# Kernel tuning notes

Hardware: AMD Instinct MI355X
Metric: run time of the kernel (lower is better)

Reference implementation:

```python
import jax, jax.numpy as jnp
import numpy as np

WS = 8
NH = 6

def _ln(x, g, b, eps=1e-5):
    m = jnp.mean(x, axis=-1, keepdims=True)
    v = jnp.var(x, axis=-1, keepdims=True)
    return (x - m) * jax.lax.rsqrt(v + eps) * g + b

def setup_inputs() -> dict:
    key = jax.random.key(0)
    ks = jax.random.split(key, 6)
    B, H, W, C = 4, 256, 256, 192
    s = 0.02
    return {
        "x": jax.random.normal(ks[0], (B, H, W, C), jnp.float32),
        "g1": jnp.ones((C,), jnp.float32),
        "b1": jnp.zeros((C,), jnp.float32),
        "w_qkv": jax.random.normal(ks[1], (C, 3 * C), jnp.float32) * s,
        "b_qkv": jnp.zeros((3 * C,), jnp.float32),
        "w_proj": jax.random.normal(ks[2], (C, C), jnp.float32) * s,
        "b_proj": jnp.zeros((C,), jnp.float32),
        "g2": jnp.ones((C,), jnp.float32),
        "b2": jnp.zeros((C,), jnp.float32),
        "w_fc1": jax.random.normal(ks[3], (C, 4 * C), jnp.float32) * s,
        "b_fc1": jnp.zeros((4 * C,), jnp.float32),
        "w_fc2": jax.random.normal(ks[4], (4 * C, C), jnp.float32) * s,
        "b_fc2": jnp.zeros((C,), jnp.float32),
    }

def reference(x, g1, b1, w_qkv, b_qkv, w_proj, b_proj, g2, b2, w_fc1, b_fc1, w_fc2, b_fc2):
    B, H, W, C = x.shape
    ws, nh = WS, NH
    hd = C // nh
    scale = hd ** -0.5
    N = ws * ws
    # window partition: (B,H,W,C) -> (B*nW, N, C). H,W divisible by ws, so pad branch is a no-op.
    xw = x.reshape(B, H // ws, ws, W // ws, ws, C).transpose(0, 1, 3, 2, 4, 5).reshape(-1, N, C)
    h = _ln(xw, g1, b1)
    qkv = h @ w_qkv + b_qkv                      # (Bn, N, 3C)
    q, k, v = jnp.split(qkv, 3, axis=-1)
    q = q.reshape(-1, N, nh, hd)
    k = k.reshape(-1, N, nh, hd)
    v = v.reshape(-1, N, nh, hd)
    attn = jax.nn.softmax(jnp.einsum('bnhd,bmhd->bhnm', q, k) * scale, axis=-1)
    o = jnp.einsum('bhnm,bmhd->bnhd', attn, v).reshape(-1, N, C)
    xw = xw + (o @ w_proj + b_proj)              # residual inside windows
    # window unpartition: (B*nW, N, C) -> (B, H, W, C)
    xo = xw.reshape(B, H // ws, W // ws, ws, ws, C).transpose(0, 1, 3, 2, 4, 5).reshape(B, H, W, C)
    h2 = _ln(xo, g2, b2)
    h2 = jax.nn.gelu(h2 @ w_fc1 + b_fc1, approximate=False) @ w_fc2 + b_fc2
    return xo + h2
```

## Files before the change

### kernel.cpp

```cpp
#include <hip/hip_runtime.h>
#include <hip/hip_bf16.h>

typedef unsigned short u16;
typedef __attribute__((ext_vector_type(8))) short short8;
typedef __attribute__((ext_vector_type(4))) short short4v;
typedef __attribute__((ext_vector_type(4))) float f32x4;

#define TOK 262144

__device__ __forceinline__ u16 f2bf(float f){
  __hip_bfloat16 h = __float2bfloat16(f);
  return *reinterpret_cast<u16*>(&h);
}

__global__ void transpose_all(const float* __restrict__ w0, u16* __restrict__ d0,
                              const float* __restrict__ w1, u16* __restrict__ d1,
                              const float* __restrict__ w2, u16* __restrict__ d2,
                              const float* __restrict__ w3, u16* __restrict__ d3)
{
  int seg = blockIdx.y;
  const float* s; u16* d; int K, N;
  if      (seg == 0){ s = w0; d = d0; K = 192; N = 576; }
  else if (seg == 1){ s = w1; d = d1; K = 192; N = 192; }
  else if (seg == 2){ s = w2; d = d2; K = 192; N = 768; }
  else              { s = w3; d = d3; K = 768; N = 192; }
  int idx = blockIdx.x * 256 + threadIdx.x;
  if (idx < K * N){
    int k = idx / N, n = idx % N;
    d[n * K + k] = f2bf(s[idx]);
  }
}

__global__ __launch_bounds__(256, 2) void win_attn(
    const float* __restrict__ x,  const float* __restrict__ g1, const float* __restrict__ b1,
    const u16* __restrict__ wqkvT, const float* __restrict__ bqkv,
    const u16* __restrict__ wprojT, const float* __restrict__ bproj,
    float* __restrict__ out)
{
  __shared__ u16 hw[64 * 200];
  __shared__ u16 wch[96 * 200];
  u16* Ql = wch;
  u16* Kl = wch + 64 * 40;
  u16* Vt = Kl  + 64 * 40;
  u16* Pl = Vt  + 32 * 72;

  const int tid = threadIdx.x, lane = tid & 63, w = tid >> 6;
  const int l15 = lane & 15, quad = lane >> 4;
  const int wid = blockIdx.x;
  const int b = wid >> 10, hy = (wid >> 5) & 31, wx = wid & 31;

  {
    int n = w * 16 + (lane >> 2), p = lane & 3;
    int hr = hy * 8 + (n >> 3), wcc = wx * 8 + (n & 7);
    size_t tg = ((size_t)(b * 256 + hr)) * 256 + wcc;
    const float* xr = x + tg * 192 + p * 48;
    float v[48];
    #pragma unroll
    for (int c = 0; c < 12; c++) *(float4*)(v + c * 4) = *(const float4*)(xr + c * 4);
    float s = 0.f, ss = 0.f;
    #pragma unroll
    for (int i = 0; i < 48; i++){ s += v[i]; ss += v[i] * v[i]; }
    s += __shfl_xor(s, 1); ss += __shfl_xor(ss, 1);
    s += __shfl_xor(s, 2); ss += __shfl_xor(ss, 2);
    float m  = s * (1.f / 192.f);
    float rs = rsqrtf(ss * (1.f / 192.f) - m * m + 1e-5f);
    #pragma unroll
    for (int c = 0; c < 12; c++){
      float4 gv = *(const float4*)(g1 + p * 48 + c * 4);
      float4 bv = *(const float4*)(b1 + p * 48 + c * 4);
      short4v t;
      t.x = (short)f2bf((v[c*4+0] - m) * rs * gv.x + bv.x);
      t.y = (short)f2bf((v[c*4+1] - m) * rs * gv.y + bv.y);
      t.z = (short)f2bf((v[c*4+2] - m) * rs * gv.z + bv.z);
      t.w = (short)f2bf((v[c*4+3] - m) * rs * gv.w + bv.w);
      *(short4v*)&hw[n * 200 + p * 48 + c * 4] = t;
    }
  }

  const int qrow = w * 16 + quad * 4;
  f32x4 oall[6][2];
  #pragma unroll
  for (int h = 0; h < 6; h++)
    #pragma unroll
    for (int nt = 0; nt < 2; nt++) oall[h][nt] = (f32x4){0.f, 0.f, 0.f, 0.f};

  #pragma unroll
  for (int head = 0; head < 6; ++head){
    __syncthreads();
    #pragma unroll
    for (int it = 0; it < 9; ++it){
      int c = tid + it * 256;
      int row = c / 24, cc = c % 24;
      int gr = (row >> 5) * 192 + head * 32 + (row & 31);
      *(uint4*)&wch[row * 200 + cc * 8] = *(const uint4*)(wqkvT + (size_t)gr * 192 + cc * 8);
    }
    __syncthreads();
    f32x4 acc[3][2];
    #pragma unroll
    for (int mat = 0; mat < 3; mat++)
      #pragma unroll
      for (int nt = 0; nt < 2; nt++) acc[mat][nt] = (f32x4){0.f, 0.f, 0.f, 0.f};
    #pragma unroll
    for (int k = 0; k < 6; k++){
      short8 af = *(const short8*)&hw[(w * 16 + l15) * 200 + k * 32 + quad * 8];
      #pragma unroll
      for (int mat = 0; mat < 3; mat++)
        #pragma unroll
        for (int nt = 0; nt < 2; nt++){
          short8 bfv = *(const short8*)&wch[(mat * 32 + nt * 16 + l15) * 200 + k * 32 + quad * 8];
          acc[mat][nt] = __builtin_amdgcn_mfma_f32_16x16x32_bf16(af, bfv, acc[mat][nt], 0, 0, 0);
        }
    }
    __syncthreads();
    #pragma unroll
    for (int nt = 0; nt < 2; nt++){
      float bq = bqkv[      head * 32 + nt * 16 + l15];
      float bk = bqkv[192 + head * 32 + nt * 16 + l15];
      float bv = bqkv[384 + head * 32 + nt * 16 + l15];
      #pragma unroll
      for (int r = 0; r < 4; r++){
        Ql[(qrow + r) * 40 + nt * 16 + l15] = f2bf(acc[0][nt][r] + bq);
        Kl[(qrow + r) * 40 + nt * 16 + l15] = f2bf(acc[1][nt][r] + bk);
        Vt[(nt * 16 + l15) * 72 + qrow + r] = f2bf(acc[2][nt][r] + bv);
      }
    }
    __syncthreads();
    short8 aq = *(const short8*)&Ql[(w * 16 + l15) * 40 + quad * 8];
    f32x4 sa[4];
    #pragma unroll
    for (int kt = 0; kt < 4; kt++){
      short8 bk8 = *(const short8*)&Kl[(kt * 16 + l15) * 40 + quad * 8];
      sa[kt] = __builtin_amdgcn_mfma_f32_16x16x32_bf16(aq, bk8, (f32x4){0.f,0.f,0.f,0.f}, 0, 0, 0);
    }
    const float scale = 0.17677669529663687f;
    float inv[4];
    #pragma unroll
    for (int r = 0; r < 4; r++){
      float s0 = sa[0][r] * scale, s1 = sa[1][r] * scale;
      float s2 = sa[2][r] * scale, s3 = sa[3][r] * scale;
      float mx = fmaxf(fmaxf(s0, s1), fmaxf(s2, s3));
      mx = fmaxf(mx, __shfl_xor(mx, 1)); mx = fmaxf(mx, __shfl_xor(mx, 2));
      mx = fmaxf(mx, __shfl_xor(mx, 4)); mx = fmaxf(mx, __shfl_xor(mx, 8));
      float p0 = __expf(s0 - mx), p1 = __expf(s1 - mx);
      float p2 = __expf(s2 - mx), p3 = __expf(s3 - mx);
      float l = p0 + p1 + p2 + p3;
      l += __shfl_xor(l, 1); l += __shfl_xor(l, 2);
      l += __shfl_xor(l, 4); l += __shfl_xor(l, 8);
      inv[r] = 1.f / l;
      Pl[(qrow + r) * 72 +      l15] = f2bf(p0);
      Pl[(qrow + r) * 72 + 16 + l15] = f2bf(p1);
      Pl[(qrow + r) * 72 + 32 + l15] = f2bf(p2);
      Pl[(qrow + r) * 72 + 48 + l15] = f2bf(p3);
    }
    f32x4 oa[2];
    oa[0] = (f32x4){0.f,0.f,0.f,0.f}; oa[1] = (f32x4){0.f,0.f,0.f,0.f};
    #pragma unroll
    for (int ks = 0; ks < 2; ks++){
      short8 ap = *(const short8*)&Pl[(w * 16 + l15) * 72 + ks * 32 + quad * 8];
      #pragma unroll
      for (int nt = 0; nt < 2; nt++){
        short8 bv8 = *(const short8*)&Vt[(nt * 16 + l15) * 72 + ks * 32 + quad * 8];
        oa[nt] = __builtin_amdgcn_mfma_f32_16x16x32_bf16(ap, bv8, oa[nt], 0, 0, 0);
      }
    }
    #pragma unroll
    for (int nt = 0; nt < 2; nt++)
      #pragma unroll
      for (int r = 0; r < 4; r++)
        oall[head][nt][r] = oa[nt][r] * inv[r];
  }

  #pragma unroll
  for (int h = 0; h < 6; h++)
    #pragma unroll
    for (int nt = 0; nt < 2; nt++)
      #pragma unroll
      for (int r = 0; r < 4; r++)
        hw[(qrow + r) * 200 + h * 32 + nt * 16 + l15] = f2bf(oall[h][nt][r]);

  f32x4 accP[12];
  #pragma unroll
  for (int nt = 0; nt < 12; nt++) accP[nt] = (f32x4){0.f,0.f,0.f,0.f};
  #pragma unroll
  for (int k = 0; k < 6; k++){
    short8 af = *(const short8*)&hw[(w * 16 + l15) * 200 + k * 32 + quad * 8];
    #pragma unroll
    for (int nt = 0; nt < 12; nt++){
      short8 bfv = *(const short8*)(wprojT + (size_t)(nt * 16 + l15) * 192 + k * 32 + quad * 8);
      accP[nt] = __builtin_amdgcn_mfma_f32_16x16x32_bf16(af, bfv, accP[nt], 0, 0, 0);
    }
  }
  #pragma unroll
  for (int r = 0; r < 4; r++){
    int nn = qrow + r;
    int hr = hy * 8 + (nn >> 3), wcc = wx * 8 + (nn & 7);
    size_t tg = ((size_t)(b * 256 + hr)) * 256 + wcc;
    #pragma unroll
    for (int nt = 0; nt < 12; nt++){
      int col = nt * 16 + l15;
      size_t idx = tg * 192 + col;
      out[idx] = accP[nt][r] + bproj[col] + x[idx];
    }
  }
}

__global__ __launch_bounds__(256, 2) void mlp_fused(
    const float* __restrict__ g2, const float* __restrict__ b2,
    const u16* __restrict__ wfc1T, const float* __restrict__ bfc1,
    const u16* __restrict__ wfc2T, const float* __restrict__ bfc2,
    float* __restrict__ io)
{
  __shared__ u16 h2t[64 * 200];
  __shared__ u16 Ut[64 * 72];
  __shared__ u16 wcs[192 * 72];

  const int tid = threadIdx.x, lane = tid & 63, w = tid >> 6;
  const int wm = w >> 1, wn = w & 1, l15 = lane & 15, quad = lane >> 4;
  const int t0 = blockIdx.x * 64;

  {
    int n = w * 16 + (lane >> 2), p = lane & 3;
    const float* xr = io + (size_t)(t0 + n) * 192 + p * 48;
    float v[48];
    #pragma unroll
    for (int c = 0; c < 12; c++) *(float4*)(v + c * 4) = *(const float4*)(xr + c * 4);
    float s = 0.f, ss = 0.f;
    #pragma unroll
    for (int i = 0; i < 48; i++){ s += v[i]; ss += v[i] * v[i]; }
    s += __shfl_xor(s, 1); ss += __shfl_xor(ss, 1);
    s += __shfl_xor(s, 2); ss += __shfl_xor(ss, 2);
    float m  = s * (1.f / 192.f);
    float rs = rsqrtf(ss * (1.f / 192.f) - m * m + 1e-5f);
    #pragma unroll
    for (int c = 0; c < 12; c++){
      float4 gv = *(const float4*)(g2 + p * 48 + c * 4);
      float4 bv = *(const float4*)(b2 + p * 48 + c * 4);
      short4v t;
      t.x = (short)f2bf((v[c*4+0] - m) * rs * gv.x + bv.x);
      t.y = (short)f2bf((v[c*4+1] - m) * rs * gv.y + bv.y);
      t.z = (short)f2bf((v[c*4+2] - m) * rs * gv.z + bv.z);
      t.w = (short)f2bf((v[c*4+3] - m) * rs * gv.w + bv.w);
      *(short4v*)&h2t[n * 200 + p * 48 + c * 4] = t;
    }
  }
  __syncthreads();

  f32x4 accO[2][6];
  #pragma unroll
  for (int mt = 0; mt < 2; mt++)
    #pragma unroll
    for (int nt = 0; nt < 6; nt++) accO[mt][nt] = (f32x4){0.f,0.f,0.f,0.f};

  for (int ch = 0; ch < 12; ++ch){
    #pragma unroll
    for (int it = 0; it < 6; ++it){
      int c = tid + it * 256;
      int row = c / 24, cc = c % 24;
      *(uint4*)&wcs[row * 200 + cc * 8] = *(const uint4*)(wfc1T + (size_t)(ch * 64 + row) * 192 + cc * 8);
    }
    __syncthreads();
    f32x4 au[2][2];
    #pragma unroll
    for (int mt = 0; mt < 2; mt++)
      #pragma unroll
      for (int nt = 0; nt < 2; nt++) au[mt][nt] = (f32x4){0.f,0.f,0.f,0.f};
    #pragma unroll
    for (int k = 0; k < 6; k++){
      short8 af0 = *(const short8*)&h2t[(wm * 32 +      l15) * 200 + k * 32 + quad * 8];
      short8 af1 = *(const short8*)&h2t[(wm * 32 + 16 + l15) * 200 + k * 32 + quad * 8];
      #pragma unroll
      for (int nt = 0; nt < 2; nt++){
        short8 bfv = *(const short8*)&wcs[(wn * 32 + nt * 16 + l15) * 200 + k * 32 + quad * 8];
        au[0][nt] = __builtin_amdgcn_mfma_f32_16x16x32_bf16(af0, bfv, au[0][nt], 0, 0, 0);
        au[1][nt] = __builtin_amdgcn_mfma_f32_16x16x32_bf16(af1, bfv, au[1][nt], 0, 0, 0);
      }
    }
    #pragma unroll
    for (int nt = 0; nt < 2; nt++){
      float bb = bfc1[ch * 64 + wn * 32 + nt * 16 + l15];
      #pragma unroll
      for (int mt = 0; mt < 2; mt++)
        #pragma unroll
        for (int r = 0; r < 4; r++){
          float u = au[mt][nt][r] + bb;
          u = 0.5f * u * (1.f + erff(u * 0.70710678118654752f));
          Ut[(wm * 32 + mt * 16 + quad * 4 + r) * 72 + wn * 32 + nt * 16 + l15] = f2bf(u);
        }
    }
    __syncthreads();
    #pragma unroll
    for (int it = 0; it < 6; ++it){
      int c = tid + it * 256;
      int row = c / 8, cc = c % 8;
      *(uint4*)&wcs[row * 72 + cc * 8] = *(const uint4*)(wfc2T + (size_t)row * 768 + ch * 64 + cc * 8);
    }
    __syncthreads();
    #pragma unroll
    for (int ks = 0; ks < 2; ks++){
      short8 af0 = *(const short8*)&Ut[(wm * 32 +      l15) * 72 + ks * 32 + quad * 8];
      short8 af1 = *(const short8*)&Ut[(wm * 32 + 16 + l15) * 72 + ks * 32 + quad * 8];
      #pragma unroll
      for (int nt = 0; nt < 6; nt++){
        short8 bfv = *(const short8*)&wcs[(wn * 96 + nt * 16 + l15) * 72 + ks * 32 + quad * 8];
        accO[0][nt] = __builtin_amdgcn_mfma_f32_16x16x32_bf16(af0, bfv, accO[0][nt], 0, 0, 0);
        accO[1][nt] = __builtin_amdgcn_mfma_f32_16x16x32_bf16(af1, bfv, accO[1][nt], 0, 0, 0);
      }
    }
    __syncthreads();
  }

  #pragma unroll
  for (int mt = 0; mt < 2; mt++)
    #pragma unroll
    for (int nt = 0; nt < 6; nt++){
      int col = wn * 96 + nt * 16 + l15;
      float bb = bfc2[col];
      #pragma unroll
      for (int r = 0; r < 4; r++){
        int row = t0 + wm * 32 + mt * 16 + quad * 4 + r;
        size_t idx = (size_t)row * 192 + col;
        io[idx] = accO[mt][nt][r] + bb + io[idx];
      }
    }
}

extern "C" void kernel_launch(void* const* d_in, const int* in_sizes, int n_in,
                              void* d_out, int out_size, void* d_ws, size_t ws_size,
                              hipStream_t stream) {
  const float* x      = (const float*)d_in[0];
  const float* g1     = (const float*)d_in[1];
  const float* b1     = (const float*)d_in[2];
  const float* w_qkv  = (const float*)d_in[3];
  const float* b_qkv  = (const float*)d_in[4];
  const float* w_proj = (const float*)d_in[5];
  const float* b_proj = (const float*)d_in[6];
  const float* g2     = (const float*)d_in[7];
  const float* b2     = (const float*)d_in[8];
  const float* w_fc1  = (const float*)d_in[9];
  const float* b_fc1  = (const float*)d_in[10];
  const float* w_fc2  = (const float*)d_in[11];
  const float* b_fc2  = (const float*)d_in[12];
  float* out = (float*)d_out;

  u16* wqkvT  = (u16*)d_ws;
  u16* wprojT = wqkvT  + 576 * 192;
  u16* wfc1T  = wprojT + 192 * 192;
  u16* wfc2T  = wfc1T  + 768 * 192;

  transpose_all<<<dim3(576, 4), 256, 0, stream>>>(w_qkv, wqkvT, w_proj, wprojT,
                                                  w_fc1, wfc1T, w_fc2, wfc2T);
  win_attn<<<4096, 256, 0, stream>>>(x, g1, b1, wqkvT, b_qkv, wprojT, b_proj, out);
  mlp_fused<<<4096, 256, 0, stream>>>(g2, b2, wfc1T, b_fc1, wfc2T, b_fc2, out);
}
```

Baseline: 993.4 us.

## Read weight fragments directly from global memory, drop LDS staging, swap erf GELU for tanh approximation

Both the attention and MLP kernels stop staging weight tiles in shared memory and instead load MFMA B-fragments straight from global memory, which relies on L1/L2 caching of the small bf16 weights. This removes the staging copies and several barriers and shrinks LDS use, and launch bounds are raised to 3 and 4 blocks per CU. The exact erf GELU is replaced with a sigmoid-form tanh approximation using exp and a fast reciprocal. The costs are more global load latency in the inner MFMA loops, tighter register limits, and a small numerical deviation from the exact GELU the reference uses.

```diff
diff --git a/kernel.cpp b/kernel.cpp
--- a/kernel.cpp
+++ b/kernel.cpp
@@ -11,6 +11,12 @@
 __device__ __forceinline__ u16 f2bf(float f){
   __hip_bfloat16 h = __float2bfloat16(f);
   return *reinterpret_cast<u16*>(&h);
+}
+
+__device__ __forceinline__ float gelu_fast(float u){
+  float uu = u * u;
+  float e = __expf(u * fmaf(uu, -0.0713548163f, -1.5957691216f));
+  return u * __builtin_amdgcn_rcpf(1.f + e);
 }
 
 __global__ void transpose_all(const float* __restrict__ w0, u16* __restrict__ d0,
@@ -31,18 +37,17 @@
   }
 }
 
-__global__ __launch_bounds__(256, 2) void win_attn(
+__global__ __launch_bounds__(256, 3) void win_attn(
     const float* __restrict__ x,  const float* __restrict__ g1, const float* __restrict__ b1,
     const u16* __restrict__ wqkvT, const float* __restrict__ bqkv,
     const u16* __restrict__ wprojT, const float* __restrict__ bproj,
     float* __restrict__ out)
 {
   __shared__ u16 hw[64 * 200];
-  __shared__ u16 wch[96 * 200];
-  u16* Ql = wch;
-  u16* Kl = wch + 64 * 40;
-  u16* Vt = Kl  + 64 * 40;
-  u16* Pl = Vt  + 32 * 72;
+  __shared__ u16 Ql[64 * 40];
+  __shared__ u16 Kl[64 * 40];
+  __shared__ u16 Vt[32 * 72];
+  __shared__ u16 Pl[64 * 72];
 
   const int tid = threadIdx.x, lane = tid & 63, w = tid >> 6;
   const int l15 = lane & 15, quad = lane >> 4;
@@ -87,14 +92,6 @@
   #pragma unroll
   for (int head = 0; head < 6; ++head){
     __syncthreads();
-    #pragma unroll
-    for (int it = 0; it < 9; ++it){
-      int c = tid + it * 256;
-      int row = c / 24, cc = c % 24;
-      int gr = (row >> 5) * 192 + head * 32 + (row & 31);
-      *(uint4*)&wch[row * 200 + cc * 8] = *(const uint4*)(wqkvT + (size_t)gr * 192 + cc * 8);
-    }
-    __syncthreads();
     f32x4 acc[3][2];
     #pragma unroll
     for (int mat = 0; mat < 3; mat++)
@@ -107,11 +104,11 @@
       for (int mat = 0; mat < 3; mat++)
         #pragma unroll
         for (int nt = 0; nt < 2; nt++){
-          short8 bfv = *(const short8*)&wch[(mat * 32 + nt * 16 + l15) * 200 + k * 32 + quad * 8];
+          short8 bfv = *(const short8*)(wqkvT +
+              (size_t)(mat * 192 + head * 32 + nt * 16 + l15) * 192 + k * 32 + quad * 8);
           acc[mat][nt] = __builtin_amdgcn_mfma_f32_16x16x32_bf16(af, bfv, acc[mat][nt], 0, 0, 0);
         }
     }
-    __syncthreads();
     #pragma unroll
     for (int nt = 0; nt < 2; nt++){
       float bq = bqkv[      head * 32 + nt * 16 + l15];
@@ -204,7 +201,7 @@
   }
 }
 
-__global__ __launch_bounds__(256, 2) void mlp_fused(
+__global__ __launch_bounds__(256, 4) void mlp_fused(
     const float* __restrict__ g2, const float* __restrict__ b2,
     const u16* __restrict__ wfc1T, const float* __restrict__ bfc1,
     const u16* __restrict__ wfc2T, const float* __restrict__ bfc2,
@@ -212,7 +209,6 @@
 {
   __shared__ u16 h2t[64 * 200];
   __shared__ u16 Ut[64 * 72];
-  __shared__ u16 wcs[192 * 72];
 
   const int tid = threadIdx.x, lane = tid & 63, w = tid >> 6;
   const int wm = w >> 1, wn = w & 1, l15 = lane & 15, quad = lane >> 4;
@@ -252,13 +248,6 @@
     for (int nt = 0; nt < 6; nt++) accO[mt][nt] = (f32x4){0.f,0.f,0.f,0.f};
 
   for (int ch = 0; ch < 12; ++ch){
-    #pragma unroll
-    for (int it = 0; it < 6; ++it){
-      int c = tid + it * 256;
-      int row = c / 24, cc = c % 24;
-      *(uint4*)&wcs[row * 200 + cc * 8] = *(const uint4*)(wfc1T + (size_t)(ch * 64 + row) * 192 + cc * 8);
-    }
-    __syncthreads();
     f32x4 au[2][2];
     #pragma unroll
     for (int mt = 0; mt < 2; mt++)
@@ -270,7 +259,8 @@
       short8 af1 = *(const short8*)&h2t[(wm * 32 + 16 + l15) * 200 + k * 32 + quad * 8];
       #pragma unroll
       for (int nt = 0; nt < 2; nt++){
-        short8 bfv = *(const short8*)&wcs[(wn * 32 + nt * 16 + l15) * 200 + k * 32 + quad * 8];
+        short8 bfv = *(const short8*)(wfc1T +
+            (size_t)(ch * 64 + wn * 32 + nt * 16 + l15) * 192 + k * 32 + quad * 8);
         au[0][nt] = __builtin_amdgcn_mfma_f32_16x16x32_bf16(af0, bfv, au[0][nt], 0, 0, 0);
         au[1][nt] = __builtin_amdgcn_mfma_f32_16x16x32_bf16(af1, bfv, au[1][nt], 0, 0, 0);
       }
@@ -283,16 +273,8 @@
         #pragma unroll
         for (int r = 0; r < 4; r++){
           float u = au[mt][nt][r] + bb;
-          u = 0.5f * u * (1.f + erff(u * 0.70710678118654752f));
-          Ut[(wm * 32 + mt * 16 + quad * 4 + r) * 72 + wn * 32 + nt * 16 + l15] = f2bf(u);
+          Ut[(wm * 32 + mt * 16 + quad * 4 + r) * 72 + wn * 32 + nt * 16 + l15] = f2bf(gelu_fast(u));
         }
-    }
-    __syncthreads();
-    #pragma unroll
-    for (int it = 0; it < 6; ++it){
-      int c = tid + it * 256;
-      int row = c / 8, cc = c % 8;
-      *(uint4*)&wcs[row * 72 + cc * 8] = *(const uint4*)(wfc2T + (size_t)row * 768 + ch * 64 + cc * 8);
     }
     __syncthreads();
     #pragma unroll
@@ -301,7 +283,8 @@
       short8 af1 = *(const short8*)&Ut[(wm * 32 + 16 + l15) * 72 + ks * 32 + quad * 8];
       #pragma unroll
       for (int nt = 0; nt < 6; nt++){
-        short8 bfv = *(const short8*)&wcs[(wn * 96 + nt * 16 + l15) * 72 + ks * 32 + quad * 8];
+        short8 bfv = *(const short8*)(wfc2T +
+            (size_t)(wn * 96 + nt * 16 + l15) * 768 + ch * 64 + ks * 32 + quad * 8);
         accO[0][nt] = __builtin_amdgcn_mfma_f32_16x16x32_bf16(af0, bfv, accO[0][nt], 0, 0, 0);
         accO[1][nt] = __builtin_amdgcn_mfma_f32_16x16x32_bf16(af1, bfv, accO[1][nt], 0, 0, 0);
       }
```

After: 1.572 ms. 1.58x slower.

## Restructure fused MLP with register-prefetched weight chunks, per-warp rows, fast GELU

Applied to the files above, without the earlier changes.

The fused MLP kernel now gives each warp 16 full token rows and loops over 24 hidden chunks of 32 instead of 12 of 64. It prefetches the next chunk of both fc1 and fc2 weights into registers while the current chunk computes, cutting the four barriers per chunk to two. Because each warp writes and reads only its own rows of the GELU tile, no barrier is needed between the two GEMMs. The exact erf GELU is replaced with a sigmoid-form tanh approximation using exp and reciprocal, which trades some accuracy for fewer ALU instructions.

```diff
diff --git a/kernel.cpp b/kernel.cpp
--- a/kernel.cpp
+++ b/kernel.cpp
@@ -11,6 +11,12 @@
 __device__ __forceinline__ u16 f2bf(float f){
   __hip_bfloat16 h = __float2bfloat16(f);
   return *reinterpret_cast<u16*>(&h);
+}
+
+__device__ __forceinline__ float gelu_fast(float u){
+  float uu = u * u;
+  float e = __expf(u * fmaf(uu, -0.0713548163f, -1.5957691216f));
+  return u * __builtin_amdgcn_rcpf(1.f + e);
 }
 
 __global__ void transpose_all(const float* __restrict__ w0, u16* __restrict__ d0,
@@ -211,12 +217,29 @@
     float* __restrict__ io)
 {
   __shared__ u16 h2t[64 * 200];
-  __shared__ u16 Ut[64 * 72];
-  __shared__ u16 wcs[192 * 72];
+  __shared__ u16 w1b[32 * 200];
+  __shared__ u16 w2b[192 * 40];
+  __shared__ u16 Ut [64 * 40];
 
   const int tid = threadIdx.x, lane = tid & 63, w = tid >> 6;
-  const int wm = w >> 1, wn = w & 1, l15 = lane & 15, quad = lane >> 4;
+  const int l15 = lane & 15, quad = lane >> 4;
   const int t0 = blockIdx.x * 64;
+
+  const int c0 = tid, c1 = tid + 256, c2 = tid + 512;
+  const int w1r0 = c0 / 24, w1c0 = c0 % 24;
+  const int w1r1 = c1 / 24, w1c1 = c1 % 24;
+  const int w1r2 = c2 / 24, w1c2 = c2 % 24;
+  const int w2r0 = c0 >> 2, w2c0 = c0 & 3;
+  const int w2r1 = c1 >> 2, w2c1 = c1 & 3;
+  const int w2r2 = c2 >> 2, w2c2 = c2 & 3;
+
+  uint4 r1a, r1b, r1c, r2a, r2b, r2c;
+  r1a = *(const uint4*)(wfc1T + (size_t)w1r0 * 192 + w1c0 * 8);
+  r1b = *(const uint4*)(wfc1T + (size_t)w1r1 * 192 + w1c1 * 8);
+  r1c = *(const uint4*)(wfc1T + (size_t)w1r2 * 192 + w1c2 * 8);
+  r2a = *(const uint4*)(wfc2T + (size_t)w2r0 * 768 + w2c0 * 8);
+  r2b = *(const uint4*)(wfc2T + (size_t)w2r1 * 768 + w2c1 * 8);
+  r2c = *(const uint4*)(wfc2T + (size_t)w2r2 * 768 + w2c2 * 8);
 
   {
     int n = w * 16 + (lane >> 2), p = lane & 3;
@@ -243,85 +266,69 @@
       *(short4v*)&h2t[n * 200 + p * 48 + c * 4] = t;
     }
   }
-  __syncthreads();
-
-  f32x4 accO[2][6];
-  #pragma unroll
-  for (int mt = 0; mt < 2; mt++)
-    #pragma unroll
-    for (int nt = 0; nt < 6; nt++) accO[mt][nt] = (f32x4){0.f,0.f,0.f,0.f};
-
-  for (int ch = 0; ch < 12; ++ch){
-    #pragma unroll
-    for (int it = 0; it < 6; ++it){
-      int c = tid + it * 256;
-      int row = c / 24, cc = c % 24;
-      *(uint4*)&wcs[row * 200 + cc * 8] = *(const uint4*)(wfc1T + (size_t)(ch * 64 + row) * 192 + cc * 8);
-    }
-    __syncthreads();
-    f32x4 au[2][2];
-    #pragma unroll
-    for (int mt = 0; mt < 2; mt++)
-      #pragma unroll
-      for (int nt = 0; nt < 2; nt++) au[mt][nt] = (f32x4){0.f,0.f,0.f,0.f};
+
+  f32x4 accO[12];
+  #pragma unroll
+  for (int nt = 0; nt < 12; nt++) accO[nt] = (f32x4){0.f,0.f,0.f,0.f};
+
+  for (int ch = 0; ch < 24; ++ch){
+    *(uint4*)&w1b[w1r0 * 200 + w1c0 * 8] = r1a;
+    *(uint4*)&w1b[w1r1 * 200 + w1c1 * 8] = r1b;
+    *(uint4*)&w1b[w1r2 * 200 + w1c2 * 8] = r1c;
+    *(uint4*)&w2b[w2r0 * 40 + w2c0 * 8] = r2a;
+    *(uint4*)&w2b[w2r1 * 40 + w2c1 * 8] = r2b;
+    *(uint4*)&w2b[w2r2 * 40 + w2c2 * 8] = r2c;
+    if (ch < 23){
+      int chn = ch + 1;
+      r1a = *(const uint4*)(wfc1T + (size_t)(chn * 32 + w1r0) * 192 + w1c0 * 8);
+      r1b = *(const uint4*)(wfc1T + (size_t)(chn * 32 + w1r1) * 192 + w1c1 * 8);
+      r1c = *(const uint4*)(wfc1T + (size_t)(chn * 32 + w1r2) * 192 + w1c2 * 8);
+      r2a = *(const uint4*)(wfc2T + (size_t)w2r0 * 768 + chn * 32 + w2c0 * 8);
+      r2b = *(const uint4*)(wfc2T + (size_t)w2r1 * 768 + chn * 32 + w2c1 * 8);
+      r2c = *(const uint4*)(wfc2T + (size_t)w2r2 * 768 + chn * 32 + w2c2 * 8);
+    }
+    __syncthreads();
+
+    f32x4 au[2];
+    au[0] = (f32x4){0.f,0.f,0.f,0.f}; au[1] = (f32x4){0.f,0.f,0.f,0.f};
     #pragma unroll
     for (int k = 0; k < 6; k++){
-      short8 af0 = *(const short8*)&h2t[(wm * 32 +      l15) * 200 + k * 32 + quad * 8];
-      short8 af1 = *(const short8*)&h2t[(wm * 32 + 16 + l15) * 200 + k * 32 + quad * 8];
+      short8 af = *(const short8*)&h2t[(w * 16 + l15) * 200 + k * 32 + quad * 8];
       #pragma unroll
       for (int nt = 0; nt < 2; nt++){
-        short8 bfv = *(const short8*)&wcs[(wn * 32 + nt * 16 + l15) * 200 + k * 32 + quad * 8];
-        au[0][nt] = __builtin_amdgcn_mfma_f32_16x16x32_bf16(af0, bfv, au[0][nt], 0, 0, 0);
-        au[1][nt] = __builtin_amdgcn_mfma_f32_16x16x32_bf16(af1, bfv, au[1][nt], 0, 0, 0);
+        short8 bfv = *(const short8*)&w1b[(nt * 16 + l15) * 200 + k * 32 + quad * 8];
+        au[nt] = __builtin_amdgcn_mfma_f32_16x16x32_bf16(af, bfv, au[nt], 0, 0, 0);
       }
     }
     #pragma unroll
     for (int nt = 0; nt < 2; nt++){
-      float bb = bfc1[ch * 64 + wn * 32 + nt * 16 + l15];
-      #pragma unroll
-      for (int mt = 0; mt < 2; mt++)
-        #pragma unroll
-        for (int r = 0; r < 4; r++){
-          float u = au[mt][nt][r] + bb;
-          u = 0.5f * u * (1.f + erff(u * 0.70710678118654752f));
-          Ut[(wm * 32 + mt * 16 + quad * 4 + r) * 72 + wn * 32 + nt * 16 + l15] = f2bf(u);
-        }
-    }
-    __syncthreads();
-    #pragma unroll
-    for (int it = 0; it < 6; ++it){
-      int c = tid + it * 256;
-      int row = c / 8, cc = c % 8;
-      *(uint4*)&wcs[row * 72 + cc * 8] = *(const uint4*)(wfc2T + (size_t)row * 768 + ch * 64 + cc * 8);
-    }
-    __syncthreads();
-    #pragma unroll
-    for (int ks = 0; ks < 2; ks++){
-      short8 af0 = *(const short8*)&Ut[(wm * 32 +      l15) * 72 + ks * 32 + quad * 8];
-      short8 af1 = *(const short8*)&Ut[(wm * 32 + 16 + l15) * 72 + ks * 32 + quad * 8];
-      #pragma unroll
-      for (int nt = 0; nt < 6; nt++){
-        short8 bfv = *(const short8*)&wcs[(wn * 96 + nt * 16 + l15) * 72 + ks * 32 + quad * 8];
-        accO[0][nt] = __builtin_amdgcn_mfma_f32_16x16x32_bf16(af0, bfv, accO[0][nt], 0, 0, 0);
-        accO[1][nt] = __builtin_amdgcn_mfma_f32_16x16x32_bf16(af1, bfv, accO[1][nt], 0, 0, 0);
+      float bb = bfc1[ch * 32 + nt * 16 + l15];
+      #pragma unroll
+      for (int r = 0; r < 4; r++){
+        float u = au[nt][r] + bb;
+        Ut[(w * 16 + quad * 4 + r) * 40 + nt * 16 + l15] = f2bf(gelu_fast(u));
       }
     }
-    __syncthreads();
-  }
-
-  #pragma unroll
-  for (int mt = 0; mt < 2; mt++)
-    #pragma unroll
-    for (int nt = 0; nt < 6; nt++){
-      int col = wn * 96 + nt * 16 + l15;
-      float bb = bfc2[col];
-      #pragma unroll
-      for (int r = 0; r < 4; r++){
-        int row = t0 + wm * 32 + mt * 16 + quad * 4 + r;
-        size_t idx = (size_t)row * 192 + col;
-        io[idx] = accO[mt][nt][r] + bb + io[idx];
-      }
-    }
+    short8 auf = *(const short8*)&Ut[(w * 16 + l15) * 40 + quad * 8];
+    #pragma unroll
+    for (int nt = 0; nt < 12; nt++){
+      short8 bfv = *(const short8*)&w2b[(nt * 16 + l15) * 40 + quad * 8];
+      accO[nt] = __builtin_amdgcn_mfma_f32_16x16x32_bf16(auf, bfv, accO[nt], 0, 0, 0);
+    }
+    __syncthreads();
+  }
+
+  #pragma unroll
+  for (int nt = 0; nt < 12; nt++){
+    int col = nt * 16 + l15;
+    float bb = bfc2[col];
+    #pragma unroll
+    for (int r = 0; r < 4; r++){
+      int row = t0 + w * 16 + quad * 4 + r;
+      size_t idx = (size_t)row * 192 + col;
+      io[idx] = accO[nt][r] + bb + io[idx];
+    }
+  }
 }
 
 extern "C" void kernel_launch(void* const* d_in, const int* in_sizes, int n_in,
```

After: 973.4 us. 2.0% less time.

## Double-buffer MLP weight chunks via direct-to-LDS loads with 32x32 MFMA and fast GELU

Applied to the files above, without the earlier changes.

Prepacks fc1/fc2 weights into padded per-chunk LDS images, then streams each next chunk with global_load_lds into a double buffer while computing the current one. This replaces the synchronous register-staged copies and most __syncthreads. MFMA switches from 16x16x32 to 32x32x16 tiles, and erf-GELU is swapped for a tanh-style exp approximation. In exchange, LDS use rises, which forces one block per CU, and the GELU approximation adds numerical error.

```diff
diff --git a/kernel.cpp b/kernel.cpp
--- a/kernel.cpp
+++ b/kernel.cpp
@@ -5,12 +5,17 @@
 typedef __attribute__((ext_vector_type(8))) short short8;
 typedef __attribute__((ext_vector_type(4))) short short4v;
 typedef __attribute__((ext_vector_type(4))) float f32x4;
-
-#define TOK 262144
+typedef __attribute__((ext_vector_type(16))) float f32x16;
 
 __device__ __forceinline__ u16 f2bf(float f){
   __hip_bfloat16 h = __float2bfloat16(f);
   return *reinterpret_cast<u16*>(&h);
+}
+
+__device__ __forceinline__ float gelu_fast(float u){
+  float uu = u * u;
+  float e = __expf(u * fmaf(uu, -0.0713548163f, -1.5957691216f));
+  return u * __builtin_amdgcn_rcpf(1.f + e);
 }
 
 __global__ void transpose_all(const float* __restrict__ w0, u16* __restrict__ d0,
@@ -19,15 +24,21 @@
                               const float* __restrict__ w3, u16* __restrict__ d3)
 {
   int seg = blockIdx.y;
-  const float* s; u16* d; int K, N;
-  if      (seg == 0){ s = w0; d = d0; K = 192; N = 576; }
-  else if (seg == 1){ s = w1; d = d1; K = 192; N = 192; }
-  else if (seg == 2){ s = w2; d = d2; K = 192; N = 768; }
-  else              { s = w3; d = d3; K = 768; N = 192; }
   int idx = blockIdx.x * 256 + threadIdx.x;
-  if (idx < K * N){
-    int k = idx / N, n = idx % N;
-    d[n * K + k] = f2bf(s[idx]);
+  if (seg == 0){
+    if (idx < 192 * 576){ int k = idx / 576, n = idx % 576; d0[n * 192 + k] = f2bf(w0[idx]); }
+  } else if (seg == 1){
+    if (idx < 192 * 192){ int k = idx / 192, n = idx % 192; d1[n * 192 + k] = f2bf(w1[idx]); }
+  } else if (seg == 2){
+    if (idx < 192 * 768){
+      int k = idx / 768, n = idx % 768;
+      d2[(size_t)(n >> 6) * 12800 + (n & 63) * 200 + k] = f2bf(w2[idx]);
+    }
+  } else {
+    if (idx < 768 * 192){
+      int k = idx / 192, n = idx % 192;
+      d3[(size_t)(k >> 6) * 13824 + n * 72 + (k & 63)] = f2bf(w3[idx]);
+    }
   }
 }
 
@@ -204,19 +215,46 @@
   }
 }
 
-__global__ __launch_bounds__(256, 2) void mlp_fused(
+__global__ __launch_bounds__(256, 1) void mlp_fused(
     const float* __restrict__ g2, const float* __restrict__ b2,
-    const u16* __restrict__ wfc1T, const float* __restrict__ bfc1,
-    const u16* __restrict__ wfc2T, const float* __restrict__ bfc2,
+    const u16* __restrict__ wfc1P, const float* __restrict__ bfc1,
+    const u16* __restrict__ wfc2P, const float* __restrict__ bfc2,
     float* __restrict__ io)
 {
   __shared__ u16 h2t[64 * 200];
+  __shared__ u16 w1s[2][64 * 200];
+  __shared__ u16 w2s[2][192 * 72];
   __shared__ u16 Ut[64 * 72];
-  __shared__ u16 wcs[192 * 72];
 
   const int tid = threadIdx.x, lane = tid & 63, w = tid >> 6;
-  const int wm = w >> 1, wn = w & 1, l15 = lane & 15, quad = lane >> 4;
+  const int wm = w >> 1, wn = w & 1;
+  const int l31 = lane & 31, half = lane >> 5;
   const int t0 = blockIdx.x * 64;
+
+  typedef const __attribute__((address_space(1))) void gv_t;
+  typedef __attribute__((address_space(3))) void lv_t;
+
+  #define STAGE(ch, buf)                                                          \
+    {                                                                             \
+      const u16* b1p = wfc1P + (size_t)(ch) * 12800;                              \
+      const u16* b2p = wfc2P + (size_t)(ch) * 13824;                              \
+      _Pragma("unroll")                                                           \
+      for (int t = 0; t < 13; ++t){                                               \
+        int j = w * 13 + t;                                                       \
+        if (j < 25)                                                               \
+          __builtin_amdgcn_global_load_lds((gv_t*)(b1p + j * 512 + lane * 8),     \
+                                           (lv_t*)&w1s[buf][j * 512], 16, 0, 0);  \
+        else                                                                      \
+          __builtin_amdgcn_global_load_lds((gv_t*)(b2p + (j-25) * 512 + lane * 8),\
+                                           (lv_t*)&w2s[buf][(j-25) * 512], 16, 0, 0);\
+      }                                                                           \
+    }
+
+  STAGE(0, 0);
+
+  float b1r[12];
+  #pragma unroll
+  for (int c = 0; c < 12; ++c) b1r[c] = bfc1[c * 64 + wn * 32 + l31];
 
   {
     int n = w * 16 + (lane >> 2), p = lane & 3;
@@ -243,85 +281,68 @@
       *(short4v*)&h2t[n * 200 + p * 48 + c * 4] = t;
     }
   }
-  __syncthreads();
-
-  f32x4 accO[2][6];
-  #pragma unroll
-  for (int mt = 0; mt < 2; mt++)
-    #pragma unroll
-    for (int nt = 0; nt < 6; nt++) accO[mt][nt] = (f32x4){0.f,0.f,0.f,0.f};
-
+
+  f32x16 accO[3];
+  #pragma unroll
+  for (int t = 0; t < 3; ++t)
+    #pragma unroll
+    for (int i = 0; i < 16; ++i) accO[t][i] = 0.f;
+
+  #pragma unroll
   for (int ch = 0; ch < 12; ++ch){
-    #pragma unroll
-    for (int it = 0; it < 6; ++it){
-      int c = tid + it * 256;
-      int row = c / 24, cc = c % 24;
-      *(uint4*)&wcs[row * 200 + cc * 8] = *(const uint4*)(wfc1T + (size_t)(ch * 64 + row) * 192 + cc * 8);
-    }
-    __syncthreads();
-    f32x4 au[2][2];
-    #pragma unroll
-    for (int mt = 0; mt < 2; mt++)
-      #pragma unroll
-      for (int nt = 0; nt < 2; nt++) au[mt][nt] = (f32x4){0.f,0.f,0.f,0.f};
-    #pragma unroll
-    for (int k = 0; k < 6; k++){
-      short8 af0 = *(const short8*)&h2t[(wm * 32 +      l15) * 200 + k * 32 + quad * 8];
-      short8 af1 = *(const short8*)&h2t[(wm * 32 + 16 + l15) * 200 + k * 32 + quad * 8];
-      #pragma unroll
-      for (int nt = 0; nt < 2; nt++){
-        short8 bfv = *(const short8*)&wcs[(wn * 32 + nt * 16 + l15) * 200 + k * 32 + quad * 8];
-        au[0][nt] = __builtin_amdgcn_mfma_f32_16x16x32_bf16(af0, bfv, au[0][nt], 0, 0, 0);
-        au[1][nt] = __builtin_amdgcn_mfma_f32_16x16x32_bf16(af1, bfv, au[1][nt], 0, 0, 0);
+    const int cur = ch & 1;
+    if (ch < 11){
+      STAGE(ch + 1, cur ^ 1);
+      asm volatile("s_waitcnt vmcnt(13)" ::: "memory");
+    } else {
+      asm volatile("s_waitcnt vmcnt(0)" ::: "memory");
+    }
+    asm volatile("s_waitcnt lgkmcnt(0)" ::: "memory");
+    __builtin_amdgcn_s_barrier();
+
+    f32x16 au;
+    #pragma unroll
+    for (int i = 0; i < 16; ++i) au[i] = 0.f;
+    #pragma unroll
+    for (int ks = 0; ks < 12; ++ks){
+      short8 af = *(const short8*)&h2t[(wm * 32 + l31) * 200 + ks * 16 + half * 8];
+      short8 bf = *(const short8*)&w1s[cur][(wn * 32 + l31) * 200 + ks * 16 + half * 8];
+      au = __builtin_amdgcn_mfma_f32_32x32x16_bf16(af, bf, au, 0, 0, 0);
+    }
+    #pragma unroll
+    for (int r = 0; r < 16; ++r){
+      int tr = (r & 3) + 8 * (r >> 2) + 4 * half;
+      float u = au[r] + b1r[ch];
+      Ut[(wm * 32 + tr) * 72 + wn * 32 + l31] = f2bf(gelu_fast(u));
+    }
+    asm volatile("s_waitcnt lgkmcnt(0)" ::: "memory");
+    __builtin_amdgcn_s_barrier();
+
+    #pragma unroll
+    for (int ks = 0; ks < 4; ++ks){
+      short8 uf = *(const short8*)&Ut[(wm * 32 + l31) * 72 + ks * 16 + half * 8];
+      #pragma unroll
+      for (int t = 0; t < 3; ++t){
+        short8 bf = *(const short8*)&w2s[cur][(wn * 96 + t * 32 + l31) * 72 + ks * 16 + half * 8];
+        accO[t] = __builtin_amdgcn_mfma_f32_32x32x16_bf16(uf, bf, accO[t], 0, 0, 0);
       }
     }
-    #pragma unroll
-    for (int nt = 0; nt < 2; nt++){
-      float bb = bfc1[ch * 64 + wn * 32 + nt * 16 + l15];
-      #pragma unroll
-      for (int mt = 0; mt < 2; mt++)
-        #pragma unroll
-        for (int r = 0; r < 4; r++){
-          float u = au[mt][nt][r] + bb;
-          u = 0.5f * u * (1.f + erff(u * 0.70710678118654752f));
-          Ut[(wm * 32 + mt * 16 + quad * 4 + r) * 72 + wn * 32 + nt * 16 + l15] = f2bf(u);
-        }
-    }
-    __syncthreads();
-    #pragma unroll
-    for (int it = 0; it < 6; ++it){
-      int c = tid + it * 256;
-      int row = c / 8, cc = c % 8;
-      *(uint4*)&wcs[row * 72 + cc * 8] = *(const uint4*)(wfc2T + (size_t)row * 768 + ch * 64 + cc * 8);
-    }
-    __syncthreads();
-    #pragma unroll
-    for (int ks = 0; ks < 2; ks++){
-      short8 af0 = *(const short8*)&Ut[(wm * 32 +      l15) * 72 + ks * 32 + quad * 8];
-      short8 af1 = *(const short8*)&Ut[(wm * 32 + 16 + l15) * 72 + ks * 32 + quad * 8];
-      #pragma unroll
-      for (int nt = 0; nt < 6; nt++){
-        short8 bfv = *(const short8*)&wcs[(wn * 96 + nt * 16 + l15) * 72 + ks * 32 + quad * 8];
-        accO[0][nt] = __builtin_amdgcn_mfma_f32_16x16x32_bf16(af0, bfv, accO[0][nt], 0, 0, 0);
-        accO[1][nt] = __builtin_amdgcn_mfma_f32_16x16x32_bf16(af1, bfv, accO[1][nt], 0, 0, 0);
-      }
-    }
-    __syncthreads();
-  }
-
-  #pragma unroll
-  for (int mt = 0; mt < 2; mt++)
-    #pragma unroll
-    for (int nt = 0; nt < 6; nt++){
-      int col = wn * 96 + nt * 16 + l15;
-      float bb = bfc2[col];
-      #pragma unroll
-      for (int r = 0; r < 4; r++){
-        int row = t0 + wm * 32 + mt * 16 + quad * 4 + r;
-        size_t idx = (size_t)row * 192 + col;
-        io[idx] = accO[mt][nt][r] + bb + io[idx];
-      }
-    }
+    asm volatile("s_waitcnt lgkmcnt(0)" ::: "memory");
+    __builtin_amdgcn_s_barrier();
+  }
+
+  #pragma unroll
+  for (int t = 0; t < 3; ++t){
+    int col = wn * 96 + t * 32 + l31;
+    float bb = bfc2[col];
+    #pragma unroll
+    for (int r = 0; r < 16; ++r){
+      int row = t0 + wm * 32 + (r & 3) + 8 * (r >> 2) + 4 * half;
+      size_t idx = (size_t)row * 192 + col;
+      io[idx] = accO[t][r] + bb + io[idx];
+    }
+  }
+  #undef STAGE
 }
 
 extern "C" void kernel_launch(void* const* d_in, const int* in_sizes, int n_in,
@@ -344,11 +365,11 @@
 
   u16* wqkvT  = (u16*)d_ws;
   u16* wprojT = wqkvT  + 576 * 192;
-  u16* wfc1T  = wprojT + 192 * 192;
-  u16* wfc2T  = wfc1T  + 768 * 192;
+  u16* wfc1P  = wprojT + 192 * 192;
+  u16* wfc2P  = wfc1P  + 12 * 12800;
 
   transpose_all<<<dim3(576, 4), 256, 0, stream>>>(w_qkv, wqkvT, w_proj, wprojT,
-                                                  w_fc1, wfc1T, w_fc2, wfc2T);
+                                                  w_fc1, wfc1P, w_fc2, wfc2P);
   win_attn<<<4096, 256, 0, stream>>>(x, g1, b1, wqkvT, b_qkv, wprojT, b_proj, out);
-  mlp_fused<<<4096, 256, 0, stream>>>(g2, b2, wfc1T, b_fc1, wfc2T, b_fc2, out);
-}
+  mlp_fused<<<4096, 256, 0, stream>>>(g2, b2, wfc1P, b_fc1, wfc2P, b_fc2, out);
+}
```

New measurement: 1.156 ms. 1.16x slower.
